# Kernel optimization log

Hardware: AMD Instinct MI355X
Metric: run time of the kernel (lower is better)

Reference implementation:

```python
import jax, jax.numpy as jnp
import numpy as np

B, C, H, W = 16, 512, 64, 64
G = 32            # factor; dynamic multinomial group count must equal factor for conv shapes to match
CG = C // G       # channels per group = 16
R = 16            # SE reduction
EPS = 1e-5


def setup_inputs() -> dict:
    key = jax.random.key(0)
    ks = jax.random.split(key, 8)
    n = lambda k, s: jax.random.normal(k, s, dtype=jnp.float32) * 0.05
    return {
        "x": jax.random.normal(ks[0], (B, C, H, W), dtype=jnp.float32),
        # 1x1 conv over cg channels (acts on concatenated pooled h/w strips)
        "w1": n(ks[1], (CG, CG)), "b1": jnp.zeros((CG,), jnp.float32),
        # 3x3 conv over cg channels
        "w3": n(ks[2], (CG, CG, 3, 3)), "b3": jnp.zeros((CG,), jnp.float32),
        # GroupNorm(num_groups=cg, num_channels=cg) affine -> per-channel over HW
        "gn_w": jnp.ones((CG,), jnp.float32), "gn_b": jnp.zeros((CG,), jnp.float32),
        # channel_gate SE (1x1 convs == dense on pooled vector)
        "cg_w1": n(ks[3], (C // R, C)), "cg_b1": jnp.zeros((C // R,), jnp.float32),
        "cg_w2": n(ks[4], (C, C // R)), "cg_b2": jnp.zeros((C,), jnp.float32),
        # global_attn SE
        "ga_w1": n(ks[5], (C // R, C)), "ga_b1": jnp.zeros((C // R,), jnp.float32),
        "ga_w2": n(ks[6], (C, C // R)), "ga_b2": jnp.zeros((C,), jnp.float32),
        # torch init is zeros(1); use 0.5 so the channel branch contributes to output
        "gamma": jnp.full((1,), 0.5, jnp.float32),
    }


def _se(t, wa, ba, wb, bb):
    # AdaptiveAvgPool2d(1) -> 1x1 conv -> ReLU -> 1x1 conv -> sigmoid
    p = t.mean((2, 3))                                  # (b, c)
    hdn = jax.nn.relu(p @ wa.T + ba)                    # (b, c//r)
    return jax.nn.sigmoid(hdn @ wb.T + bb)[:, :, None, None]


def reference(x, w1, b1, w3, b3, gn_w, gn_b, cg_w1, cg_b1, cg_w2, cg_b2,
              ga_w1, ga_b1, ga_w2, ga_b2, gamma):
    b, c, h, w = x.shape
    g, cg = G, c // G
    gx = x.reshape(b * g, cg, h, w)

    # coordinate pooling: (bg, cg, h, 1) and (bg, cg, w, 1)
    xh = gx.mean(3, keepdims=True)
    xw = gx.mean(2, keepdims=True).transpose(0, 1, 3, 2)
    hw = jnp.einsum('oc,bcld->bold', w1, jnp.concatenate([xh, xw], axis=2))
    hw = hw + b1[None, :, None, None]
    xh, xw = hw[:, :, :h], hw[:, :, h:]

    # gated map + per-channel GroupNorm (num_groups == num_channels)
    x1 = gx * jax.nn.sigmoid(xh) * jax.nn.sigmoid(xw.transpose(0, 1, 3, 2))
    mu = x1.mean((2, 3), keepdims=True)
    var = x1.var((2, 3), keepdims=True)
    x1 = (x1 - mu) * jax.lax.rsqrt(var + EPS)
    x1 = x1 * gn_w[None, :, None, None] + gn_b[None, :, None, None]

    # 3x3 conv branch
    x2 = jax.lax.conv_general_dilated(gx, w3, (1, 1), 'SAME',
                                      dimension_numbers=('NCHW', 'OIHW', 'NCHW'))
    x2 = x2 + b3[None, :, None, None]

    # pooled-softmax cross attention: (bg,1,cg) @ (bg,cg,hw)
    a11 = jax.nn.softmax(x1.mean((2, 3)), axis=-1)      # (bg, cg)
    a21 = jax.nn.softmax(x2.mean((2, 3)), axis=-1)
    wv = jnp.einsum('bc,bchw->bhw', a11, x2) + jnp.einsum('bc,bchw->bhw', a21, x1)
    spatial = (gx * jax.nn.sigmoid(wv)[:, None]).reshape(b, c, h, w)

    channel = x * _se(x, cg_w1, cg_b1, cg_w2, cg_b2)
    fused = spatial + gamma * channel
    return fused * _se(fused, ga_w1, ga_b1, ga_w2, ga_b2)
```

## Files before the change

kernel.cpp:

```cpp
#include <hip/hip_runtime.h>
#include <math.h>

#define EPS 1e-5f

typedef float __attribute__((ext_vector_type(4))) floatx4;

__device__ __forceinline__ float sigmoidf_(float v){ return 1.0f/(1.0f+expf(-v)); }
__device__ __forceinline__ unsigned short f2bf_(float f){
    unsigned int u = __builtin_bit_cast(unsigned int, f);
    return (unsigned short)((u + 0x8000u) >> 16);
}
__device__ __forceinline__ float bf2f_(unsigned short s){
    unsigned int u = ((unsigned int)s) << 16;
    return __builtin_bit_cast(float, u);
}

__global__ __launch_bounds__(1024) __attribute__((amdgpu_waves_per_eu(4,4)))
void kAB_L(const float* __restrict__ x,
    const float* __restrict__ w1, const float* __restrict__ b1,
    const float* __restrict__ w3, const float* __restrict__ b3,
    const float* __restrict__ gn_w, const float* __restrict__ gn_b,
    float* __restrict__ chansum, float* __restrict__ sigbuf, float* __restrict__ p2part)
{
    const int bg = blockIdx.x;
    const int tid = threadIdx.x;
    const int w = tid >> 6;
    const int lane = tid & 63;

    __shared__ unsigned short xls[16][64][64];
    __shared__ float rs_s[16][64], cs_s[16][64];
    __shared__ float sh_s[16][64], sw_s[16][64];
    __shared__ float chs_s[16], corn_s[16][4], mu_s[16], rstd_s[16];
    __shared__ float w1s[256], b1s[16];
    __shared__ float regs[144], m2[16];
    __shared__ float weff_s[144], alpha_s[16], cb_s[2];
    __shared__ float red_s[16][16];

    if (tid < 256) w1s[tid] = w1[tid];
    if (tid < 16)  b1s[tid] = b1[tid];

    const float* xc = x + (((size_t)bg<<4) + w)*4096;
    const float4* xc4 = (const float4*)xc;

    {
        float c0=0.f,c1=0.f,c2=0.f,c3=0.f;
        #pragma unroll
        for (int it=0; it<16; ++it){
            float4 v = xc4[it*64 + lane];
            int row = it*4 + (lane>>4);
            int cb4 = (lane&15)*4;
            uint2 pk;
            pk.x = (unsigned int)f2bf_(v.x) | ((unsigned int)f2bf_(v.y)<<16);
            pk.y = (unsigned int)f2bf_(v.z) | ((unsigned int)f2bf_(v.w)<<16);
            *(uint2*)&xls[w][row][cb4] = pk;
            float rsum = v.x+v.y+v.z+v.w;
            rsum += __shfl_xor(rsum,1); rsum += __shfl_xor(rsum,2);
            rsum += __shfl_xor(rsum,4); rsum += __shfl_xor(rsum,8);
            if ((lane&15)==0) rs_s[w][row] = rsum;
            c0+=v.x; c1+=v.y; c2+=v.z; c3+=v.w;
        }
        c0 += __shfl_xor(c0,16); c0 += __shfl_xor(c0,32);
        c1 += __shfl_xor(c1,16); c1 += __shfl_xor(c1,32);
        c2 += __shfl_xor(c2,16); c2 += __shfl_xor(c2,32);
        c3 += __shfl_xor(c3,16); c3 += __shfl_xor(c3,32);
        float tsum = c0+c1+c2+c3;
        tsum += __shfl_xor(tsum,1); tsum += __shfl_xor(tsum,2);
        tsum += __shfl_xor(tsum,4); tsum += __shfl_xor(tsum,8);
        if (lane < 16){
            cs_s[w][lane*4+0]=c0; cs_s[w][lane*4+1]=c1;
            cs_s[w][lane*4+2]=c2; cs_s[w][lane*4+3]=c3;
        }
        if (lane==0){
            chs_s[w]=tsum;
            chansum[(bg<<4)+w]=tsum;
            corn_s[w][0]=xc[0]; corn_s[w][1]=xc[63];
            corn_s[w][2]=xc[4032]; corn_s[w][3]=xc[4095];
        }
    }
    __syncthreads();

    {
        int p  = tid & 127;
        int o0 = tid >> 7;
        bool isrow = (p < 64);
        int pp = p & 63;
        float cat[16];
        #pragma unroll
        for (int cc=0; cc<16; ++cc)
            cat[cc] = (isrow ? rs_s[cc][pp] : cs_s[cc][pp]) * (1.0f/64.0f);
        #pragma unroll
        for (int t2=0; t2<2; ++t2){
            int o = o0 + t2*8;
            float acc = b1s[o];
            #pragma unroll
            for (int cc=0; cc<16; ++cc) acc += w1s[o*16+cc]*cat[cc];
            float sg = sigmoidf_(acc);
            if (isrow) sh_s[o][pp]=sg;
            else       sw_s[o][pp]=sg;
        }
    }
    if (tid < 145){
        float a11[16];
        {
            float mx = gn_b[0];
            #pragma unroll
            for (int i=1;i<16;++i) mx = fmaxf(mx, gn_b[i]);
            float s=0.f;
            #pragma unroll
            for (int i=0;i<16;++i){ a11[i]=expf(gn_b[i]-mx); s+=a11[i]; }
            float inv = 1.0f/s;
            #pragma unroll
            for (int i=0;i<16;++i) a11[i]*=inv;
        }
        if (tid<144){
            float acc=0.f;
            #pragma unroll
            for (int o=0;o<16;++o) acc += a11[o]*w3[o*144+tid];
            weff_s[tid]=acc;
        } else {
            float acc=0.f;
            #pragma unroll
            for (int o=0;o<16;++o) acc += a11[o]*b3[o];
            cb_s[1]=acc;
        }
    }
    __syncthreads();

    {
        int jb = (lane&15)*4;
        float sw0=sw_s[w][jb], sw1=sw_s[w][jb+1], sw2=sw_s[w][jb+2], sw3=sw_s[w][jb+3];
        float s1=0.f, s2=0.f;
        #pragma unroll
        for (int it=0; it<16; ++it){
            int row = it*4 + (lane>>4);
            uint2 pk = *(const uint2*)&xls[w][row][jb];
            float vx = bf2f_((unsigned short)(pk.x & 0xFFFF));
            float vy = bf2f_((unsigned short)(pk.x >> 16));
            float vz = bf2f_((unsigned short)(pk.y & 0xFFFF));
            float vw = bf2f_((unsigned short)(pk.y >> 16));
            float si = sh_s[w][row];
            float a0=vx*si*sw0, a1=vy*si*sw1, a2=vz*si*sw2, a3=vw*si*sw3;
            s1 += a0+a1+a2+a3;
            s2 += a0*a0+a1*a1+a2*a2+a3*a3;
        }
        #pragma unroll
        for (int mm=1;mm<64;mm<<=1){ s1+=__shfl_xor(s1,mm); s2+=__shfl_xor(s2,mm); }
        if (lane==0){
            float mu = s1*(1.0f/4096.0f);
            float var = s2*(1.0f/4096.0f) - mu*mu;
            mu_s[w]=mu; rstd_s[w]=rsqrtf(var+EPS);
        }
    }
    if (tid >= 896 && tid < 1040){  }
    __syncthreads();

    if (tid < 144){
        int c = tid/9, k = tid - c*9, ky = k/3, kx = k - ky*3;
        float r = chs_s[c];
        if (ky==0) r -= rs_s[c][63];
        if (ky==2) r -= rs_s[c][0];
        if (kx==0) r -= cs_s[c][63];
        if (kx==2) r -= cs_s[c][0];
        if (ky!=1 && kx!=1) r += corn_s[c][((ky==0)?2:0)+((kx==0)?1:0)];
        regs[tid] = r;
    }
    __syncthreads();
    if (tid < 256){
        int c = tid >> 4, t = tid & 15;
        float s = 0.f;
        #pragma unroll
        for (int q=0;q<9;++q) s += w3[c*144 + t + q*16] * regs[t + q*16];
        s += __shfl_xor(s,1); s += __shfl_xor(s,2);
        s += __shfl_xor(s,4); s += __shfl_xor(s,8);
        if (t==0) m2[c] = b3[c] + s*(1.0f/4096.0f);
    }
    __syncthreads();
    if (tid < 16){
        float m2v = m2[tid];
        float mx = m2v;
        #pragma unroll
        for (int mm=1; mm<16; mm<<=1) mx = fmaxf(mx, __shfl_xor(mx, mm));
        float e = expf(m2v - mx);
        float ssum = e;
        #pragma unroll
        for (int mm=1; mm<16; mm<<=1) ssum += __shfl_xor(ssum, mm);
        float a21v = e / ssum;
        float rst = rstd_s[tid];
        alpha_s[tid] = a21v * gn_w[tid] * rst;
        float term = a21v * (gn_b[tid] - gn_w[tid]*rst*mu_s[tid]);
        #pragma unroll
        for (int mm=1; mm<16; mm<<=1) term += __shfl_xor(term, mm);
        if (tid==0) cb_s[0] = term;
    }
    __syncthreads();

    {
        const int j = lane;
        const int r0 = __builtin_amdgcn_readfirstlane(4*w);
        const float cstv = cb_s[0] + cb_s[1];

        float A0[4], A1[4], A2[4], G[4];
        float keep[16][4];
        #pragma unroll
        for (int r=0;r<4;++r){ A0[r]=0.f; A1[r]=0.f; A2[r]=0.f; G[r]=0.f; }

        #pragma unroll
        for (int c=0;c<16;++c){
            float w0=weff_s[c*9+0], w1_=weff_s[c*9+1], w2=weff_s[c*9+2];
            float w3_=weff_s[c*9+3], w4=weff_s[c*9+4], w5=weff_s[c*9+5];
            float w6=weff_s[c*9+6], w7=weff_s[c*9+7], w8=weff_s[c*9+8];
            float alc = alpha_s[c];
            float swv = sw_s[c][j];
            float v[6];
            #pragma unroll
            for (int k=0;k<6;++k){
                int t = r0 - 1 + k;
                int tc = t < 0 ? 0 : (t > 63 ? 63 : t);
                float val = bf2f_(xls[c][tc][j]);
                v[k] = (t >= 0 && t < 64) ? val : 0.f;
            }
            #pragma unroll
            for (int r=0;r<4;++r) keep[c][r] = v[r+1];
            #pragma unroll
            for (int k=0;k<6;++k){
                if (k<=3){ A0[k]+=w0*v[k]; A1[k]+=w1_*v[k]; A2[k]+=w2*v[k]; }
                if (k>=1 && k<=4){
                    A0[k-1]+=w3_*v[k]; A1[k-1]+=w4*v[k]; A2[k-1]+=w5*v[k];
                    float u = alc * sh_s[c][r0+k-1];
                    G[k-1] += u * (swv * v[k]);
                }
                if (k>=2){ A0[k-2]+=w6*v[k]; A1[k-2]+=w7*v[k]; A2[k-2]+=w8*v[k]; }
            }
        }

        float sg[4];
        #pragma unroll
        for (int r=0;r<4;++r){
            float l = __shfl_up(A0[r], 1);
            if (j==0) l = 0.f;
            float rr = __shfl_down(A2[r], 1);
            if (j==63) rr = 0.f;
            float s = sigmoidf_(l + A1[r] + rr + G[r] + cstv);
            sg[r] = s;
            sigbuf[(size_t)bg*4096 + (r0+r)*64 + j] = s;
        }

        #pragma unroll
        for (int c=0;c<16;++c){
            float acc = keep[c][0]*sg[0] + keep[c][1]*sg[1]
                      + keep[c][2]*sg[2] + keep[c][3]*sg[3];
            #pragma unroll
            for (int mm=1;mm<64;mm<<=1) acc += __shfl_xor(acc, mm);
            if (j==0) red_s[w][c] = acc;
        }
    }
    __syncthreads();
    if (tid<16){
        float tot = 0.f;
        #pragma unroll
        for (int ww=0;ww<16;++ww) tot += red_s[ww][tid];
        p2part[(bg<<4)+tid] = tot;
    }
}

__global__ __launch_bounds__(512) void k_se12(const float* __restrict__ chansum,
    const float* __restrict__ p2part, const float* __restrict__ gamma,
    const float* __restrict__ cg_w1, const float* __restrict__ cg_b1,
    const float* __restrict__ cg_w2, const float* __restrict__ cg_b2,
    const float* __restrict__ ga_w1, const float* __restrict__ ga_b1,
    const float* __restrict__ ga_w2, const float* __restrict__ ga_b2,
    float* __restrict__ se1, float* __restrict__ se2)
{
    int b = blockIdx.x, tid = threadIdx.x;
    __shared__ float pv[512];
    __shared__ float hdn[32];
    __shared__ float se1_s[512];
    const int n = tid >> 4;
    const int cch = tid & 15;

    float cs_v = chansum[b*512+tid];
    pv[tid] = cs_v*(1.0f/4096.0f);
    __syncthreads();
    {
        const float* wr = cg_w1 + n*512 + cch*32;
        const float* pvc = pv + cch*32;
        float acc = 0.f;
        #pragma unroll
        for (int k=0;k<32;++k) acc += wr[k]*pvc[k];
        acc += __shfl_xor(acc,1); acc += __shfl_xor(acc,2);
        acc += __shfl_xor(acc,4); acc += __shfl_xor(acc,8);
        if (cch==0) hdn[n] = fmaxf(acc + cg_b1[n], 0.0f);
    }
    __syncthreads();
    {
        float acc = cg_b2[tid];
        const float* wr = cg_w2 + tid*32;
        #pragma unroll
        for (int k=0;k<32;++k) acc += wr[k]*hdn[k];
        float s1v = sigmoidf_(acc);
        se1_s[tid] = s1v;
        se1[b*512+tid] = s1v;
    }
    __syncthreads();
    {
        float praw = p2part[b*512+tid];
        float g0 = gamma[0];
        pv[tid] = (praw + g0*se1_s[tid]*cs_v) * (1.0f/4096.0f);
    }
    __syncthreads();
    {
        const float* wr = ga_w1 + n*512 + cch*32;
        const float* pvc = pv + cch*32;
        float acc = 0.f;
        #pragma unroll
        for (int k=0;k<32;++k) acc += wr[k]*pvc[k];
        acc += __shfl_xor(acc,1); acc += __shfl_xor(acc,2);
        acc += __shfl_xor(acc,4); acc += __shfl_xor(acc,8);
        if (cch==0) hdn[n] = fmaxf(acc + ga_b1[n], 0.0f);
    }
    __syncthreads();
    {
        float acc = ga_b2[tid];
        const float* wr = ga_w2 + tid*32;
        #pragma unroll
        for (int k=0;k<32;++k) acc += wr[k]*hdn[k];
        se2[b*512+tid] = sigmoidf_(acc);
    }
}

__global__ __launch_bounds__(256) void k7_out(const float* __restrict__ x,
    const float* __restrict__ sigbuf, const float* __restrict__ se1,
    const float* __restrict__ se2, const float* __restrict__ gamma,
    float* __restrict__ out)
{
    const floatx4* x4 = (const floatx4*)x;
    const floatx4* s4 = (const floatx4*)sigbuf;
    floatx4* o4 = (floatx4*)out;
    float g0 = gamma[0];
    int idx = blockIdx.x*256 + threadIdx.x;
    int stride = gridDim.x*256;
    for (int g4 = idx; g4 < 8388608; g4 += stride){
        int e = g4 << 2;
        int bC = e >> 12;
        int pix4 = g4 & 1023;
        int bg = bC >> 4;
        floatx4 xv = x4[g4];
        floatx4 sg = s4[bg*1024 + pix4];
        float f1 = g0*se1[bC];
        float s2v = se2[bC];
        floatx4 ov;
        ov.x = xv.x*(sg.x+f1)*s2v;
        ov.y = xv.y*(sg.y+f1)*s2v;
        ov.z = xv.z*(sg.z+f1)*s2v;
        ov.w = xv.w*(sg.w+f1)*s2v;
        __builtin_nontemporal_store(ov, &o4[g4]);
    }
}

extern "C" void kernel_launch(void* const* d_in, const int* in_sizes, int n_in,
                              void* d_out, int out_size, void* d_ws, size_t ws_size,
                              hipStream_t stream)
{
    const float* x     = (const float*)d_in[0];
    const float* w1    = (const float*)d_in[1];
    const float* b1    = (const float*)d_in[2];
    const float* w3    = (const float*)d_in[3];
    const float* b3    = (const float*)d_in[4];
    const float* gn_w  = (const float*)d_in[5];
    const float* gn_b  = (const float*)d_in[6];
    const float* cg_w1 = (const float*)d_in[7];
    const float* cg_b1 = (const float*)d_in[8];
    const float* cg_w2 = (const float*)d_in[9];
    const float* cg_b2 = (const float*)d_in[10];
    const float* ga_w1 = (const float*)d_in[11];
    const float* ga_b1 = (const float*)d_in[12];
    const float* ga_w2 = (const float*)d_in[13];
    const float* ga_b2 = (const float*)d_in[14];
    const float* gamma = (const float*)d_in[15];
    float* out = (float*)d_out;
    float* ws  = (float*)d_ws;

    float* chansum = ws + 0;
    float* p2part  = ws + 8192;
    float* se1     = ws + 16384;
    float* se2     = ws + 24576;
    float* sigbuf  = ws + 32768;

    kAB_L<<<512,1024,0,stream>>>(x, w1, b1, w3, b3, gn_w, gn_b, chansum, sigbuf, p2part);
    k_se12<<<16,512,0,stream>>>(chansum, p2part, gamma, cg_w1, cg_b1, cg_w2, cg_b2,
                                ga_w1, ga_b1, ga_w2, ga_b2, se1, se2);
    k7_out<<<8192,256,0,stream>>>(x, sigbuf, se1, se2, gamma, out);
}
```

Before: 117.9 us.

## Fuse GroupNorm statistics pass into the 3x3 conv loop and trim barriers

Drops the separate pass over the bf16 LDS tile that computed per-channel GroupNorm mean and variance. Each wave now accumulates partial sums for its own four rows inside the 3x3 conv loop, and a small reduction combines them later. The regs computation moves to otherwise idle threads so two barriers can be removed. In exchange, the gated term G is computed in a second loop that rereads LDS, and the per-channel wave shuffle reductions add work inside the conv loop.

```diff
diff --git a/kernel.cpp b/kernel.cpp
--- a/kernel.cpp
+++ b/kernel.cpp
@@ -30,11 +30,11 @@
     __shared__ unsigned short xls[16][64][64];
     __shared__ float rs_s[16][64], cs_s[16][64];
     __shared__ float sh_s[16][64], sw_s[16][64];
-    __shared__ float chs_s[16], corn_s[16][4], mu_s[16], rstd_s[16];
+    __shared__ float chs_s[16], corn_s[16][4];
     __shared__ float w1s[256], b1s[16];
     __shared__ float regs[144], m2[16];
     __shared__ float weff_s[144], alpha_s[16], cb_s[2];
-    __shared__ float red_s[16][16];
+    __shared__ float red_s[16][16], s1r[16][16], s2r[16][16];
 
     if (tid < 256) w1s[tid] = w1[tid];
     if (tid < 16)  b1s[tid] = b1[tid];
@@ -124,92 +124,31 @@
             cb_s[1]=acc;
         }
     }
-    __syncthreads();
-
-    {
-        int jb = (lane&15)*4;
-        float sw0=sw_s[w][jb], sw1=sw_s[w][jb+1], sw2=sw_s[w][jb+2], sw3=sw_s[w][jb+3];
-        float s1=0.f, s2=0.f;
-        #pragma unroll
-        for (int it=0; it<16; ++it){
-            int row = it*4 + (lane>>4);
-            uint2 pk = *(const uint2*)&xls[w][row][jb];
-            float vx = bf2f_((unsigned short)(pk.x & 0xFFFF));
-            float vy = bf2f_((unsigned short)(pk.x >> 16));
-            float vz = bf2f_((unsigned short)(pk.y & 0xFFFF));
-            float vw = bf2f_((unsigned short)(pk.y >> 16));
-            float si = sh_s[w][row];
-            float a0=vx*si*sw0, a1=vy*si*sw1, a2=vz*si*sw2, a3=vw*si*sw3;
-            s1 += a0+a1+a2+a3;
-            s2 += a0*a0+a1*a1+a2*a2+a3*a3;
-        }
-        #pragma unroll
-        for (int mm=1;mm<64;mm<<=1){ s1+=__shfl_xor(s1,mm); s2+=__shfl_xor(s2,mm); }
-        if (lane==0){
-            float mu = s1*(1.0f/4096.0f);
-            float var = s2*(1.0f/4096.0f) - mu*mu;
-            mu_s[w]=mu; rstd_s[w]=rsqrtf(var+EPS);
-        }
-    }
-    if (tid >= 896 && tid < 1040){  }
-    __syncthreads();
-
-    if (tid < 144){
-        int c = tid/9, k = tid - c*9, ky = k/3, kx = k - ky*3;
+    if (tid >= 256 && tid < 400){
+        int q = tid - 256;
+        int c = q/9, k = q - c*9, ky = k/3, kx = k - ky*3;
         float r = chs_s[c];
         if (ky==0) r -= rs_s[c][63];
         if (ky==2) r -= rs_s[c][0];
         if (kx==0) r -= cs_s[c][63];
         if (kx==2) r -= cs_s[c][0];
         if (ky!=1 && kx!=1) r += corn_s[c][((ky==0)?2:0)+((kx==0)?1:0)];
-        regs[tid] = r;
-    }
-    __syncthreads();
-    if (tid < 256){
-        int c = tid >> 4, t = tid & 15;
-        float s = 0.f;
-        #pragma unroll
-        for (int q=0;q<9;++q) s += w3[c*144 + t + q*16] * regs[t + q*16];
-        s += __shfl_xor(s,1); s += __shfl_xor(s,2);
-        s += __shfl_xor(s,4); s += __shfl_xor(s,8);
-        if (t==0) m2[c] = b3[c] + s*(1.0f/4096.0f);
-    }
-    __syncthreads();
-    if (tid < 16){
-        float m2v = m2[tid];
-        float mx = m2v;
-        #pragma unroll
-        for (int mm=1; mm<16; mm<<=1) mx = fmaxf(mx, __shfl_xor(mx, mm));
-        float e = expf(m2v - mx);
-        float ssum = e;
-        #pragma unroll
-        for (int mm=1; mm<16; mm<<=1) ssum += __shfl_xor(ssum, mm);
-        float a21v = e / ssum;
-        float rst = rstd_s[tid];
-        alpha_s[tid] = a21v * gn_w[tid] * rst;
-        float term = a21v * (gn_b[tid] - gn_w[tid]*rst*mu_s[tid]);
-        #pragma unroll
-        for (int mm=1; mm<16; mm<<=1) term += __shfl_xor(term, mm);
-        if (tid==0) cb_s[0] = term;
-    }
-    __syncthreads();
-
+        regs[q] = r;
+    }
+    __syncthreads();
+
+    float A0[4], A1[4], A2[4];
     {
         const int j = lane;
         const int r0 = __builtin_amdgcn_readfirstlane(4*w);
-        const float cstv = cb_s[0] + cb_s[1];
-
-        float A0[4], A1[4], A2[4], G[4];
-        float keep[16][4];
-        #pragma unroll
-        for (int r=0;r<4;++r){ A0[r]=0.f; A1[r]=0.f; A2[r]=0.f; G[r]=0.f; }
+        #pragma unroll
+        for (int r=0;r<4;++r){ A0[r]=0.f; A1[r]=0.f; A2[r]=0.f; }
 
         #pragma unroll
         for (int c=0;c<16;++c){
             float w0=weff_s[c*9+0], w1_=weff_s[c*9+1], w2=weff_s[c*9+2];
             float w3_=weff_s[c*9+3], w4=weff_s[c*9+4], w5=weff_s[c*9+5];
             float w6=weff_s[c*9+6], w7=weff_s[c*9+7], w8=weff_s[c*9+8];
-            float alc = alpha_s[c];
             float swv = sw_s[c][j];
             float v[6];
             #pragma unroll
@@ -220,19 +159,81 @@
                 v[k] = (t >= 0 && t < 64) ? val : 0.f;
             }
             #pragma unroll
-            for (int r=0;r<4;++r) keep[c][r] = v[r+1];
-            #pragma unroll
             for (int k=0;k<6;++k){
                 if (k<=3){ A0[k]+=w0*v[k]; A1[k]+=w1_*v[k]; A2[k]+=w2*v[k]; }
-                if (k>=1 && k<=4){
-                    A0[k-1]+=w3_*v[k]; A1[k-1]+=w4*v[k]; A2[k-1]+=w5*v[k];
-                    float u = alc * sh_s[c][r0+k-1];
-                    G[k-1] += u * (swv * v[k]);
-                }
+                if (k>=1 && k<=4){ A0[k-1]+=w3_*v[k]; A1[k-1]+=w4*v[k]; A2[k-1]+=w5*v[k]; }
                 if (k>=2){ A0[k-2]+=w6*v[k]; A1[k-2]+=w7*v[k]; A2[k-2]+=w8*v[k]; }
             }
-        }
-
+            float a0_ = v[1]*sh_s[c][r0+0]*swv;
+            float a1_ = v[2]*sh_s[c][r0+1]*swv;
+            float a2_ = v[3]*sh_s[c][r0+2]*swv;
+            float a3_ = v[4]*sh_s[c][r0+3]*swv;
+            float s1c = a0_+a1_+a2_+a3_;
+            float s2c = a0_*a0_+a1_*a1_+a2_*a2_+a3_*a3_;
+            #pragma unroll
+            for (int mm=1;mm<64;mm<<=1){ s1c+=__shfl_xor(s1c,mm); s2c+=__shfl_xor(s2c,mm); }
+            if (j==0){ s1r[w][c]=s1c; s2r[w][c]=s2c; }
+        }
+    }
+    __syncthreads();
+
+    if (tid < 256){
+        int c = tid >> 4, t = tid & 15;
+        float s = 0.f;
+        #pragma unroll
+        for (int q=0;q<9;++q) s += w3[c*144 + t + q*16] * regs[t + q*16];
+        s += __shfl_xor(s,1); s += __shfl_xor(s,2);
+        s += __shfl_xor(s,4); s += __shfl_xor(s,8);
+        if (t==0) m2[c] = b3[c] + s*(1.0f/4096.0f);
+    }
+    __syncthreads();
+    if (tid < 16){
+        float S1=0.f, S2=0.f;
+        #pragma unroll
+        for (int ww=0; ww<16; ++ww){ S1 += s1r[ww][tid]; S2 += s2r[ww][tid]; }
+        float mu = S1*(1.0f/4096.0f);
+        float var = S2*(1.0f/4096.0f) - mu*mu;
+        float rst = rsqrtf(var+EPS);
+        float m2v = m2[tid];
+        float mx = m2v;
+        #pragma unroll
+        for (int mm=1; mm<16; mm<<=1) mx = fmaxf(mx, __shfl_xor(mx, mm));
+        float e = expf(m2v - mx);
+        float ssum = e;
+        #pragma unroll
+        for (int mm=1; mm<16; mm<<=1) ssum += __shfl_xor(ssum, mm);
+        float a21v = e / ssum;
+        alpha_s[tid] = a21v * gn_w[tid] * rst;
+        float term = a21v * (gn_b[tid] - gn_w[tid]*rst*mu);
+        #pragma unroll
+        for (int mm=1; mm<16; mm<<=1) term += __shfl_xor(term, mm);
+        if (tid==0) cb_s[0] = term;
+    }
+    __syncthreads();
+
+    {
+        const int j = lane;
+        const int r0 = __builtin_amdgcn_readfirstlane(4*w);
+        const float cstv = cb_s[0] + cb_s[1];
+
+        float G[4];
+        float keep[16][4];
+        #pragma unroll
+        for (int r=0;r<4;++r) G[r]=0.f;
+        #pragma unroll
+        for (int c=0;c<16;++c){
+            float alc = alpha_s[c];
+            float swv = sw_s[c][j];
+            float k0 = bf2f_(xls[c][r0+0][j]);
+            float k1 = bf2f_(xls[c][r0+1][j]);
+            float k2 = bf2f_(xls[c][r0+2][j]);
+            float k3 = bf2f_(xls[c][r0+3][j]);
+            keep[c][0]=k0; keep[c][1]=k1; keep[c][2]=k2; keep[c][3]=k3;
+            G[0] += (alc*sh_s[c][r0+0]) * (swv*k0);
+            G[1] += (alc*sh_s[c][r0+1]) * (swv*k1);
+            G[2] += (alc*sh_s[c][r0+2]) * (swv*k2);
+            G[3] += (alc*sh_s[c][r0+3]) * (swv*k3);
+        }
         float sg[4];
         #pragma unroll
         for (int r=0;r<4;++r){
@@ -244,7 +245,6 @@
             sg[r] = s;
             sigbuf[(size_t)bg*4096 + (r0+r)*64 + j] = s;
         }
-
         #pragma unroll
         for (int c=0;c<16;++c){
             float acc = keep[c][0]*sg[0] + keep[c][1]*sg[1]
```

Measured after the change: 208.3 us. 1.77x slower.
